# Kernel tuning notes

Hardware: AMD Instinct MI355X
Metric: run time of the kernel (lower is better)

The kernel has to match this reference:

```python
import jax, jax.numpy as jnp
import numpy as np

B, T, C = 4, 2048, 1024
H, D = 16, 64           # num_heads, head_size
R = D // 2              # rotary_ndims = 32


def _make_rope(T, R):
    # RotaryEmbedding(dim=R): inv_freq over arange(0, R, 2)
    inv_freq = 1.0 / (10000.0 ** (np.arange(0, R, 2, dtype=np.float32) / R))
    t = np.arange(T, dtype=np.float32)
    freqs = np.einsum('i,j->ij', t, inv_freq)        # [T, R/2]
    emb = np.concatenate([freqs, freqs], axis=-1)    # [T, R]
    return jnp.asarray(np.stack([np.cos(emb), np.sin(emb)]), dtype=jnp.float32)  # [2, T, R]


def setup_inputs() -> dict:
    key = jax.random.key(0)
    ks = jax.random.split(key, 10)
    s = 1.0 / np.sqrt(C)
    inp = {
        'x': jax.random.normal(ks[0], (B, T, C), dtype=jnp.float32),
        'RoPE': _make_rope(T, R),
        'key_padding_mask': jax.random.randint(ks[1], (B, T), 0, 2, dtype=jnp.int32),
        'Wq': jax.random.normal(ks[2], (C, C), dtype=jnp.float32) * s,
        'bq': jnp.zeros((C,), dtype=jnp.float32),
        'Wk': jax.random.normal(ks[3], (C, C), dtype=jnp.float32) * s,
        'bk': jnp.zeros((C,), dtype=jnp.float32),
        'Wv': jax.random.normal(ks[4], (C, C), dtype=jnp.float32) * s,
        'bv': jnp.zeros((C,), dtype=jnp.float32),
        'Wo': jax.random.normal(ks[5], (C, C), dtype=jnp.float32) * s,
        'bo': jnp.zeros((C,), dtype=jnp.float32),
    }
    return inp


def _rotate_half(x):
    x1, x2 = x[..., : x.shape[-1] // 2], x[..., x.shape[-1] // 2:]
    return jnp.concatenate([-x2, x1], axis=-1)


def reference(x, RoPE, key_padding_mask, Wq, bq, Wk, bk, Wv, bv, Wo, bo):
    Bx, Tx, Cx = x.shape
    # projections -> [B, H, T, D]
    def proj(W, b):
        return (x @ W.T + b).reshape(Bx, Tx, H, D).transpose(0, 2, 1, 3)
    q, k, v = proj(Wq, bq), proj(Wk, bk), proj(Wv, bv)

    # partial rotary: first R dims rotated, rest passed through
    q_rot, q_pass = q[..., :R], q[..., R:]
    k_rot, k_pass = k[..., :R], k[..., R:]
    cos, sin = RoPE[0][:Tx], RoPE[1][:Tx]            # [T, R]
    q_rot = q_rot * cos + _rotate_half(q_rot) * sin
    k_rot = k_rot * cos + _rotate_half(k_rot) * sin
    q = jnp.concatenate([q_rot, q_pass], axis=-1)
    k = jnp.concatenate([k_rot, k_pass], axis=-1)

    att = jnp.einsum('bhqd,bhkd->bhqk', q, k) * (1.0 / np.sqrt(D))
    mask = key_padding_mask[:, None, None, :]        # [B,1,1,T]
    att = jnp.where(mask == 0, jnp.asarray(-1e30, att.dtype), att)
    att = jax.nn.softmax(att, axis=-1)
    out = jnp.einsum('bhqk,bhkd->bhqd', att, v)      # [B,H,T,D]
    out = out.transpose(0, 2, 1, 3).reshape(Bx, Tx, Cx)
    return out @ Wo.T + bo
```

## Files before the change

kernel.cpp:

```cpp
#include <hip/hip_runtime.h>
#include <stdint.h>


typedef __attribute__((ext_vector_type(8))) short bf16x8;
typedef __attribute__((ext_vector_type(4))) float f32x4;
typedef __attribute__((ext_vector_type(4))) short short4v;
typedef __attribute__((ext_vector_type(4))) float float4v;
typedef __attribute__((ext_vector_type(2))) uint32_t uint2v;

#define MFMA16(a, b, c) __builtin_amdgcn_mfma_f32_16x16x32_bf16((a), (b), (c), 0, 0, 0)

#if __has_builtin(__builtin_amdgcn_exp2f)
#define FEXP(x) __builtin_amdgcn_exp2f(x)
#define QSCALE 0.18033688011112042f
#else
#define FEXP(x) __expf(x)
#define QSCALE 0.125f
#endif

static __device__ __forceinline__ short f2bf(float f) {
  union { float fv; uint32_t u; } v; v.fv = f;
  uint32_t r = v.u + 0x7FFFu + ((v.u >> 16) & 1u);
  return (short)(r >> 16);
}

static __device__ __forceinline__ uint32_t pack_trunc(float a, float b) {
  union { float f; uint32_t u; } ua, ub;
  ua.f = a; ub.f = b;
#if __has_builtin(__builtin_amdgcn_perm)
  return __builtin_amdgcn_perm(ub.u, ua.u, 0x07060302u);
#else
  return (ub.u & 0xFFFF0000u) | (ua.u >> 16);
#endif
}

typedef __attribute__((address_space(1))) void as1_void;
typedef __attribute__((address_space(3))) void as3_void;
static __device__ __forceinline__ void gld_lds16(const void* g, void* l) {
  __builtin_amdgcn_global_load_lds((as1_void*)g, (as3_void*)l, 16, 0, 0);
}

__global__ __launch_bounds__(256) void cvt_kernel(
    const float* x, const float* wq, const float* wk, const float* wv,
    const float* wo,
    short* xb, short* wqb, short* wkb, short* wvb, short* wob) {
  int64_t g = (int64_t)blockIdx.x * 256 + threadIdx.x;
  const int64_t NX = 8388608 / 4, NW = 1048576 / 4;
  const float* src;
  short* dst;
  int64_t i;
  if (g < NX)               { src = x;  dst = xb;  i = g; }
  else if (g < NX + NW)     { src = wq; dst = wqb; i = g - NX; }
  else if (g < NX + 2 * NW) { src = wk; dst = wkb; i = g - NX - NW; }
  else if (g < NX + 3 * NW) { src = wv; dst = wvb; i = g - NX - 2 * NW; }
  else                      { src = wo; dst = wob; i = g - NX - 3 * NW; }
  float4 v = ((const float4*)src)[i];
  short4v o;
  o[0] = f2bf(v.x); o[1] = f2bf(v.y); o[2] = f2bf(v.z); o[3] = f2bf(v.w);
  *(short4v*)&dst[i * 4] = o;
}

__global__ __launch_bounds__(256) void qkv_gemm(
    const short* __restrict__ Xb,
    const short* __restrict__ Wq, const short* __restrict__ Wk,
    const short* __restrict__ Wv,
    const float* __restrict__ bq, const float* __restrict__ bk,
    const float* __restrict__ bv,
    const float* __restrict__ rope, const int* __restrict__ mask,
    short* __restrict__ Qh, short* __restrict__ Kh, short* __restrict__ Vt) {
  __shared__ __align__(16) short As[128 * 32];
  __shared__ __align__(16) short Bs[128 * 32];

  const int t = threadIdx.x;
  const int lane = t & 63;
  const int wave = t >> 6;
  const int c = lane & 15;
  const int quad = lane >> 4;
  const int m0 = blockIdx.x * 128;
  const int n0 = blockIdx.y * 128;
  const int mat = blockIdx.z;
  const short* Wg = (mat == 0) ? Wq : (mat == 1) ? Wk : Wv;
  const float* bias = (mat == 0) ? bq : (mat == 1) ? bk : bv;

  f32x4 zero4 = {0.f, 0.f, 0.f, 0.f};
  f32x4 acc[4][4];
#pragma unroll
  for (int i = 0; i < 4; ++i)
#pragma unroll
    for (int j = 0; j < 4; ++j) acc[i][j] = zero4;

  const int wm = wave & 1, wn = wave >> 1;

  const int srow = t >> 2;
  const int slc = (t & 3) ^ (srow & 3);
  const short* gA = Xb + (size_t)(m0 + srow) * 1024 + slc * 8;
  const short* gB = Wg + (size_t)(n0 + srow) * 1024 + slc * 8;
  short* lA = &As[t * 8];
  short* lB = &Bs[t * 8];

  for (int k0 = 0; k0 < 1024; k0 += 32) {
    gld_lds16(gA + k0, lA);
    gld_lds16(gA + k0 + 65536, lA + 2048);
    gld_lds16(gB + k0, lB);
    gld_lds16(gB + k0 + 65536, lB + 2048);
    __syncthreads();

    bf16x8 af[4], bfr[4];
#pragma unroll
    for (int i = 0; i < 4; ++i) {
      int mr = wm * 64 + i * 16 + c;
      af[i] = *(const bf16x8*)&As[mr * 32 + ((quad ^ (mr & 3)) * 8)];
      int nr = wn * 64 + i * 16 + c;
      bfr[i] = *(const bf16x8*)&Bs[nr * 32 + ((quad ^ (nr & 3)) * 8)];
    }
#pragma unroll
    for (int i = 0; i < 4; ++i)
#pragma unroll
      for (int j = 0; j < 4; ++j) acc[i][j] = MFMA16(af[i], bfr[j], acc[i][j]);
    __syncthreads();
  }

  const int nb = n0 + wn * 64;
  const int hcol = nb >> 6;
  float bj[4];
#pragma unroll
  for (int j = 0; j < 4; ++j) bj[j] = bias[nb + j * 16 + c];
  const int bidx = m0 >> 11;
  const int tbase = (m0 & 2047) + wm * 64 + quad * 4;
  const int* mrow = mask + bidx * 2048;

  if (mat < 2) {
    short* Og = (mat == 0) ? Qh : Kh;
    size_t hb = (size_t)(bidx * 16 + hcol) * 2048;
#pragma unroll
    for (int i = 0; i < 4; ++i) {
#pragma unroll
      for (int r = 0; r < 4; ++r) {
        int tp = tbase + i * 16 + r;
        float f = (mat == 0) ? QSCALE : (mrow[tp] ? 1.0f : 0.0f);
        float cosv = rope[tp * 32 + c];
        float sinv = rope[65536 + tp * 32 + c];
        float v0 = acc[i][0][r] + bj[0];
        float v1 = acc[i][1][r] + bj[1];
        float v2 = acc[i][2][r] + bj[2];
        float v3 = acc[i][3][r] + bj[3];
        size_t base = (hb + tp) * 64;
        Og[base + c]      = f2bf((v0 * cosv - v1 * sinv) * f);
        Og[base + 16 + c] = f2bf((v1 * cosv + v0 * sinv) * f);
        Og[base + 32 + c] = f2bf(v2 * f);
        Og[base + 48 + c] = f2bf(v3 * f);
      }
    }
  } else {
    size_t hb = (size_t)(bidx * 16 + hcol) * 64;
#pragma unroll
    for (int i = 0; i < 4; ++i) {
      int tp = tbase + i * 16;
      int4 mv = *(const int4*)&mrow[tp];
      float fr[4];
      fr[0] = mv.x ? 1.f : 0.f; fr[1] = mv.y ? 1.f : 0.f;
      fr[2] = mv.z ? 1.f : 0.f; fr[3] = mv.w ? 1.f : 0.f;
#pragma unroll
      for (int j = 0; j < 4; ++j) {
        short4v pv;
#pragma unroll
        for (int r = 0; r < 4; ++r) pv[r] = f2bf((acc[i][j][r] + bj[j]) * fr[r]);
        size_t base = (hb + j * 16 + c) * 2048 + tp;
        *(short4v*)&Vt[base] = pv;
      }
    }
  }
}

__global__ __launch_bounds__(256, 4) void attn_kernel(
    const short* __restrict__ Qh, const short* __restrict__ Kh,
    const short* __restrict__ Vt, const int* __restrict__ mask,
    short* __restrict__ Og) {
  __shared__ __align__(16) short Ks[64 * 64];
  __shared__ __align__(16) short Vs[64 * 64];
  __shared__ __align__(16) short Pl[4][32 * 64];
  __shared__ float nmw[4];

  const int t = threadIdx.x;
  const int lane = t & 63;
  const int wave = t >> 6;
  const int c = lane & 15;
  const int quad = lane >> 4;
  const int qt = blockIdx.x;
  const int bh = blockIdx.y;
  const int bidx = bh >> 4;
  const short* Qg = Qh + ((size_t)bh * 2048 + qt * 128) * 64;
  const short* Kg = Kh + (size_t)bh * 2048 * 64;
  const short* Vg = Vt + (size_t)bh * 64 * 2048;

  {
    const int4* mr = (const int4*)(mask + bidx * 2048);
    int4 a = mr[t * 2], b = mr[t * 2 + 1];
    int cnt = (a.x == 0) + (a.y == 0) + (a.z == 0) + (a.w == 0) +
              (b.x == 0) + (b.y == 0) + (b.z == 0) + (b.w == 0);
    cnt += __shfl_xor(cnt, 1);  cnt += __shfl_xor(cnt, 2);
    cnt += __shfl_xor(cnt, 4);  cnt += __shfl_xor(cnt, 8);
    cnt += __shfl_xor(cnt, 16); cnt += __shfl_xor(cnt, 32);
    if (lane == 0) nmw[wave] = (float)cnt;
  }

  bf16x8 qf[2][2];
#pragma unroll
  for (int ks = 0; ks < 2; ++ks)
#pragma unroll
    for (int it = 0; it < 2; ++it)
      qf[ks][it] =
          *(const bf16x8*)&Qg[(wave * 32 + it * 16 + c) * 64 + ks * 32 + quad * 8];

  f32x4 zero4 = {0.f, 0.f, 0.f, 0.f};
  f32x4 O[4][2];
#pragma unroll
  for (int dt = 0; dt < 4; ++dt)
#pragma unroll
    for (int it = 0; it < 2; ++it) O[dt][it] = zero4;
  float l[2] = {0.f, 0.f};

  const int krow0 = t >> 3;
  const int klc = (t & 7) ^ (krow0 & 7);
  const short* gk0 = Kg + (size_t)krow0 * 64 + klc * 8;
  const short* gv0 = Vg + (size_t)krow0 * 2048 + klc * 8;
  short* Pw = &Pl[wave][0];

  for (int c0 = 0; c0 < 2048; c0 += 64) {
    gld_lds16(gk0 + (size_t)c0 * 64, &Ks[t * 8]);
    gld_lds16(gk0 + (size_t)(c0 + 32) * 64, &Ks[t * 8 + 2048]);
    gld_lds16(gv0 + c0, &Vs[t * 8]);
    gld_lds16(gv0 + c0 + 32 * 2048, &Vs[t * 8 + 2048]);
    __syncthreads();

    f32x4 St[4][2];
#pragma unroll
    for (int jt = 0; jt < 4; ++jt) { St[jt][0] = zero4; St[jt][1] = zero4; }
#pragma unroll
    for (int ks = 0; ks < 2; ++ks)
#pragma unroll
      for (int jt = 0; jt < 4; ++jt) {
        bf16x8 ak =
            *(const bf16x8*)&Ks[(jt * 16 + c) * 64 + (((4 * ks + quad) ^ (c & 7)) * 8)];
        St[jt][0] = MFMA16(ak, qf[ks][0], St[jt][0]);
        St[jt][1] = MFMA16(ak, qf[ks][1], St[jt][1]);
      }

#pragma unroll
    for (int it = 0; it < 2; ++it) {
#pragma unroll
      for (int jt = 0; jt < 4; ++jt) {
        float p0 = FEXP(St[jt][it][0]);
        float p1 = FEXP(St[jt][it][1]);
        float p2 = FEXP(St[jt][it][2]);
        float p3 = FEXP(St[jt][it][3]);
        l[it] += (p0 + p1) + (p2 + p3);
        uint2v pk;
        pk[0] = pack_trunc(p0, p1);
        pk[1] = pack_trunc(p2, p3);
        *(uint2v*)&Pw[(it * 16 + c) * 64 +
                      (((jt * 2 + (quad >> 1)) ^ (c & 7)) * 8) + (quad & 1) * 4] = pk;
      }
    }
    asm volatile("s_waitcnt lgkmcnt(0)" ::: "memory");

#pragma unroll
    for (int ks = 0; ks < 2; ++ks) {
      bf16x8 bp0 = *(const bf16x8*)&Pw[c * 64 + (((ks * 4 + quad) ^ (c & 7)) * 8)];
      bf16x8 bp1 =
          *(const bf16x8*)&Pw[(16 + c) * 64 + (((ks * 4 + quad) ^ (c & 7)) * 8)];
#pragma unroll
      for (int dt = 0; dt < 4; ++dt) {
        bf16x8 av =
            *(const bf16x8*)&Vs[(dt * 16 + c) * 64 + (((4 * ks + quad) ^ (c & 7)) * 8)];
        O[dt][0] = MFMA16(av, bp0, O[dt][0]);
        O[dt][1] = MFMA16(av, bp1, O[dt][1]);
      }
    }
    __syncthreads();
  }

  float nm = nmw[0] + nmw[1] + nmw[2] + nmw[3];
#pragma unroll
  for (int it = 0; it < 2; ++it) {
    float li = l[it];
    li += __shfl_xor(li, 16);
    li += __shfl_xor(li, 32);
    float inv = 1.0f / (li - nm);
    int tq = qt * 128 + wave * 32 + it * 16 + c;
    size_t rb = ((size_t)bidx * 2048 + tq) * 1024 + (size_t)(bh & 15) * 64;
#pragma unroll
    for (int dt = 0; dt < 4; ++dt) {
      short4v ov;
#pragma unroll
      for (int r = 0; r < 4; ++r) ov[r] = f2bf(O[dt][it][r] * inv);
      *(short4v*)&Og[rb + dt * 16 + quad * 4] = ov;
    }
  }
}

__global__ __launch_bounds__(256) void out_gemm(
    const short* __restrict__ Ab, const short* __restrict__ Wob,
    const float* __restrict__ bo, float* __restrict__ out) {
  __shared__ __align__(16) short As[128 * 32];
  __shared__ __align__(16) short Bs[128 * 32];

  const int t = threadIdx.x;
  const int lane = t & 63;
  const int wave = t >> 6;
  const int c = lane & 15;
  const int quad = lane >> 4;
  const int m0 = blockIdx.x * 128;
  const int n0 = blockIdx.y * 128;

  f32x4 zero4 = {0.f, 0.f, 0.f, 0.f};
  f32x4 acc[4][4];
#pragma unroll
  for (int i = 0; i < 4; ++i)
#pragma unroll
    for (int j = 0; j < 4; ++j) acc[i][j] = zero4;

  const int wm = wave & 1, wn = wave >> 1;
  const int srow = t >> 2;
  const int slc = (t & 3) ^ (srow & 3);
  const short* gA = Ab + (size_t)(m0 + srow) * 1024 + slc * 8;
  const short* gB = Wob + (size_t)(n0 + srow) * 1024 + slc * 8;
  short* lA = &As[t * 8];
  short* lB = &Bs[t * 8];

  for (int k0 = 0; k0 < 1024; k0 += 32) {
    gld_lds16(gA + k0, lA);
    gld_lds16(gA + k0 + 65536, lA + 2048);
    gld_lds16(gB + k0, lB);
    gld_lds16(gB + k0 + 65536, lB + 2048);
    __syncthreads();

    bf16x8 af[4], bfr[4];
#pragma unroll
    for (int i = 0; i < 4; ++i) {
      int mr = wm * 64 + i * 16 + c;
      af[i] = *(const bf16x8*)&As[mr * 32 + ((quad ^ (mr & 3)) * 8)];
      int nr = wn * 64 + i * 16 + c;
      bfr[i] = *(const bf16x8*)&Bs[nr * 32 + ((quad ^ (nr & 3)) * 8)];
    }
#pragma unroll
    for (int i = 0; i < 4; ++i)
#pragma unroll
      for (int j = 0; j < 4; ++j) acc[i][j] = MFMA16(af[i], bfr[j], acc[i][j]);
    __syncthreads();
  }

  const int nb = n0 + wn * 64;
  float bj[4];
#pragma unroll
  for (int j = 0; j < 4; ++j) bj[j] = bo[nb + j * 16 + c];
#pragma unroll
  for (int i = 0; i < 4; ++i) {
    int m = m0 + wm * 64 + i * 16 + quad * 4;
#pragma unroll
    for (int r = 0; r < 4; ++r) {
      float* orow = out + (size_t)(m + r) * 1024 + nb;
      orow[c]      = acc[i][0][r] + bj[0];
      orow[16 + c] = acc[i][1][r] + bj[1];
      orow[32 + c] = acc[i][2][r] + bj[2];
      orow[48 + c] = acc[i][3][r] + bj[3];
    }
  }
}

extern "C" void kernel_launch(void* const* d_in, const int* in_sizes, int n_in,
                              void* d_out, int out_size, void* d_ws,
                              size_t ws_size, hipStream_t stream) {
  const float* x    = (const float*)d_in[0];
  const float* rope = (const float*)d_in[1];
  const int*   mask = (const int*)d_in[2];
  const float* Wq   = (const float*)d_in[3];
  const float* bq   = (const float*)d_in[4];
  const float* Wk   = (const float*)d_in[5];
  const float* bk   = (const float*)d_in[6];
  const float* Wv   = (const float*)d_in[7];
  const float* bv   = (const float*)d_in[8];
  const float* Wo   = (const float*)d_in[9];
  const float* bo   = (const float*)d_in[10];
  float* out = (float*)d_out;

  char* ws = (char*)d_ws;
  short* xb  = (short*)(ws);
  short* wqb = (short*)(ws + 16777216);
  short* wkb = (short*)(ws + 18874368);
  short* wvb = (short*)(ws + 20971520);
  short* wob = (short*)(ws + 23068672);
  short* Qh  = (short*)(ws + 25198592);
  short* Kh  = (short*)(ws + 41975808);
  short* Vt  = (short*)(ws + 58753024);
  short* att = xb;

  cvt_kernel<<<12288, 256, 0, stream>>>(x, Wq, Wk, Wv, Wo, xb, wqb, wkb, wvb,
                                        wob);
  qkv_gemm<<<dim3(64, 8, 3), 256, 0, stream>>>(xb, wqb, wkb, wvb, bq, bk, bv,
                                               rope, mask, Qh, Kh, Vt);
  attn_kernel<<<dim3(16, 64), 256, 0, stream>>>(Qh, Kh, Vt, mask, att);
  out_gemm<<<dim3(64, 8), 256, 0, stream>>>(att, wob, bo, out);
}
```

Before: 292.0 us.

## Deepen GEMM K-tiles, shrink out_gemm M-tile, compute softmax row sums via MFMA

The QKV GEMM now stages 64-wide K slices with an 8-way XOR swizzle, which halves the number of barriers per K loop. The output GEMM switches to 64x128 tiles with a 4x2 MFMA accumulator per wave and doubles the grid, giving more blocks to fill the CUs. In attention, the per-thread softmax denominator sums and their cross-lane shuffles are replaced by an extra MFMA against a ones vector, and the S computation is split into two explicit passes. The cost is more LDS per block and extra MFMA work, and the row sums now come from the bf16-truncated P values instead of the fp32 exponentials.

```diff
diff --git a/kernel.cpp b/kernel.cpp
--- a/kernel.cpp
+++ b/kernel.cpp
@@ -5,7 +5,6 @@
 typedef __attribute__((ext_vector_type(8))) short bf16x8;
 typedef __attribute__((ext_vector_type(4))) float f32x4;
 typedef __attribute__((ext_vector_type(4))) short short4v;
-typedef __attribute__((ext_vector_type(4))) float float4v;
 typedef __attribute__((ext_vector_type(2))) uint32_t uint2v;
 
 #define MFMA16(a, b, c) __builtin_amdgcn_mfma_f32_16x16x32_bf16((a), (b), (c), 0, 0, 0)
@@ -68,8 +67,8 @@
     const float* __restrict__ bv,
     const float* __restrict__ rope, const int* __restrict__ mask,
     short* __restrict__ Qh, short* __restrict__ Kh, short* __restrict__ Vt) {
-  __shared__ __align__(16) short As[128 * 32];
-  __shared__ __align__(16) short Bs[128 * 32];
+  __shared__ __align__(16) short As[128 * 64];
+  __shared__ __align__(16) short Bs[128 * 64];
 
   const int t = threadIdx.x;
   const int lane = t & 63;
@@ -91,32 +90,34 @@
 
   const int wm = wave & 1, wn = wave >> 1;
 
-  const int srow = t >> 2;
-  const int slc = (t & 3) ^ (srow & 3);
-  const short* gA = Xb + (size_t)(m0 + srow) * 1024 + slc * 8;
-  const short* gB = Wg + (size_t)(n0 + srow) * 1024 + slc * 8;
-  short* lA = &As[t * 8];
-  short* lB = &Bs[t * 8];
-
-  for (int k0 = 0; k0 < 1024; k0 += 32) {
-    gld_lds16(gA + k0, lA);
-    gld_lds16(gA + k0 + 65536, lA + 2048);
-    gld_lds16(gB + k0, lB);
-    gld_lds16(gB + k0 + 65536, lB + 2048);
-    __syncthreads();
-
-    bf16x8 af[4], bfr[4];
-#pragma unroll
-    for (int i = 0; i < 4; ++i) {
-      int mr = wm * 64 + i * 16 + c;
-      af[i] = *(const bf16x8*)&As[mr * 32 + ((quad ^ (mr & 3)) * 8)];
-      int nr = wn * 64 + i * 16 + c;
-      bfr[i] = *(const bf16x8*)&Bs[nr * 32 + ((quad ^ (nr & 3)) * 8)];
-    }
-#pragma unroll
-    for (int i = 0; i < 4; ++i)
-#pragma unroll
-      for (int j = 0; j < 4; ++j) acc[i][j] = MFMA16(af[i], bfr[j], acc[i][j]);
+  const int srow = t >> 3;
+  const int schunk = (t & 7) ^ (srow & 7);
+  const short* gA = Xb + (size_t)(m0 + srow) * 1024 + schunk * 8;
+  const short* gB = Wg + (size_t)(n0 + srow) * 1024 + schunk * 8;
+
+  for (int k0 = 0; k0 < 1024; k0 += 64) {
+#pragma unroll
+    for (int cc = 0; cc < 4; ++cc) {
+      gld_lds16(gA + k0 + cc * 32 * 1024, &As[cc * 2048 + t * 8]);
+      gld_lds16(gB + k0 + cc * 32 * 1024, &Bs[cc * 2048 + t * 8]);
+    }
+    __syncthreads();
+
+#pragma unroll
+    for (int sl = 0; sl < 2; ++sl) {
+      bf16x8 af[4], bfr[4];
+#pragma unroll
+      for (int i = 0; i < 4; ++i) {
+        int mr = wm * 64 + i * 16 + c;
+        af[i] = *(const bf16x8*)&As[mr * 64 + (((sl * 4 + quad) ^ (mr & 7)) * 8)];
+        int nr = wn * 64 + i * 16 + c;
+        bfr[i] = *(const bf16x8*)&Bs[nr * 64 + (((sl * 4 + quad) ^ (nr & 7)) * 8)];
+      }
+#pragma unroll
+      for (int i = 0; i < 4; ++i)
+#pragma unroll
+        for (int j = 0; j < 4; ++j) acc[i][j] = MFMA16(af[i], bfr[j], acc[i][j]);
+    }
     __syncthreads();
   }
 
@@ -212,13 +213,16 @@
       qf[ks][it] =
           *(const bf16x8*)&Qg[(wave * 32 + it * 16 + c) * 64 + ks * 32 + quad * 8];
 
+  const bf16x8 ones = {0x3F80, 0x3F80, 0x3F80, 0x3F80,
+                       0x3F80, 0x3F80, 0x3F80, 0x3F80};
+
   f32x4 zero4 = {0.f, 0.f, 0.f, 0.f};
   f32x4 O[4][2];
 #pragma unroll
   for (int dt = 0; dt < 4; ++dt)
 #pragma unroll
     for (int it = 0; it < 2; ++it) O[dt][it] = zero4;
-  float l[2] = {0.f, 0.f};
+  f32x4 Ol[2] = {zero4, zero4};
 
   const int krow0 = t >> 3;
   const int klc = (t & 7) ^ (krow0 & 7);
@@ -235,16 +239,19 @@
 
     f32x4 St[4][2];
 #pragma unroll
-    for (int jt = 0; jt < 4; ++jt) { St[jt][0] = zero4; St[jt][1] = zero4; }
-#pragma unroll
-    for (int ks = 0; ks < 2; ++ks)
-#pragma unroll
-      for (int jt = 0; jt < 4; ++jt) {
-        bf16x8 ak =
-            *(const bf16x8*)&Ks[(jt * 16 + c) * 64 + (((4 * ks + quad) ^ (c & 7)) * 8)];
-        St[jt][0] = MFMA16(ak, qf[ks][0], St[jt][0]);
-        St[jt][1] = MFMA16(ak, qf[ks][1], St[jt][1]);
-      }
+    for (int jt = 0; jt < 4; ++jt) {
+      bf16x8 ak =
+          *(const bf16x8*)&Ks[(jt * 16 + c) * 64 + ((quad ^ (c & 7)) * 8)];
+      St[jt][0] = MFMA16(ak, qf[0][0], zero4);
+      St[jt][1] = MFMA16(ak, qf[0][1], zero4);
+    }
+#pragma unroll
+    for (int jt = 0; jt < 4; ++jt) {
+      bf16x8 ak =
+          *(const bf16x8*)&Ks[(jt * 16 + c) * 64 + (((4 + quad) ^ (c & 7)) * 8)];
+      St[jt][0] = MFMA16(ak, qf[1][0], St[jt][0]);
+      St[jt][1] = MFMA16(ak, qf[1][1], St[jt][1]);
+    }
 
 #pragma unroll
     for (int it = 0; it < 2; ++it) {
@@ -254,7 +261,6 @@
         float p1 = FEXP(St[jt][it][1]);
         float p2 = FEXP(St[jt][it][2]);
         float p3 = FEXP(St[jt][it][3]);
-        l[it] += (p0 + p1) + (p2 + p3);
         uint2v pk;
         pk[0] = pack_trunc(p0, p1);
         pk[1] = pack_trunc(p2, p3);
@@ -269,6 +275,8 @@
       bf16x8 bp0 = *(const bf16x8*)&Pw[c * 64 + (((ks * 4 + quad) ^ (c & 7)) * 8)];
       bf16x8 bp1 =
           *(const bf16x8*)&Pw[(16 + c) * 64 + (((ks * 4 + quad) ^ (c & 7)) * 8)];
+      Ol[0] = MFMA16(ones, bp0, Ol[0]);
+      Ol[1] = MFMA16(ones, bp1, Ol[1]);
 #pragma unroll
       for (int dt = 0; dt < 4; ++dt) {
         bf16x8 av =
@@ -283,10 +291,7 @@
   float nm = nmw[0] + nmw[1] + nmw[2] + nmw[3];
 #pragma unroll
   for (int it = 0; it < 2; ++it) {
-    float li = l[it];
-    li += __shfl_xor(li, 16);
-    li += __shfl_xor(li, 32);
-    float inv = 1.0f / (li - nm);
+    float inv = 1.0f / (Ol[it][0] - nm);
     int tq = qt * 128 + wave * 32 + it * 16 + c;
     size_t rb = ((size_t)bidx * 2048 + tq) * 1024 + (size_t)(bh & 15) * 64;
 #pragma unroll
@@ -302,68 +307,72 @@
 __global__ __launch_bounds__(256) void out_gemm(
     const short* __restrict__ Ab, const short* __restrict__ Wob,
     const float* __restrict__ bo, float* __restrict__ out) {
-  __shared__ __align__(16) short As[128 * 32];
-  __shared__ __align__(16) short Bs[128 * 32];
+  __shared__ __align__(16) short As[64 * 64];
+  __shared__ __align__(16) short Bs[128 * 64];
 
   const int t = threadIdx.x;
   const int lane = t & 63;
   const int wave = t >> 6;
   const int c = lane & 15;
   const int quad = lane >> 4;
-  const int m0 = blockIdx.x * 128;
+  const int m0 = blockIdx.x * 64;
   const int n0 = blockIdx.y * 128;
 
   f32x4 zero4 = {0.f, 0.f, 0.f, 0.f};
-  f32x4 acc[4][4];
-#pragma unroll
-  for (int i = 0; i < 4; ++i)
-#pragma unroll
-    for (int j = 0; j < 4; ++j) acc[i][j] = zero4;
-
-  const int wm = wave & 1, wn = wave >> 1;
-  const int srow = t >> 2;
-  const int slc = (t & 3) ^ (srow & 3);
-  const short* gA = Ab + (size_t)(m0 + srow) * 1024 + slc * 8;
-  const short* gB = Wob + (size_t)(n0 + srow) * 1024 + slc * 8;
-  short* lA = &As[t * 8];
-  short* lB = &Bs[t * 8];
-
-  for (int k0 = 0; k0 < 1024; k0 += 32) {
-    gld_lds16(gA + k0, lA);
-    gld_lds16(gA + k0 + 65536, lA + 2048);
-    gld_lds16(gB + k0, lB);
-    gld_lds16(gB + k0 + 65536, lB + 2048);
-    __syncthreads();
-
-    bf16x8 af[4], bfr[4];
-#pragma unroll
-    for (int i = 0; i < 4; ++i) {
-      int mr = wm * 64 + i * 16 + c;
-      af[i] = *(const bf16x8*)&As[mr * 32 + ((quad ^ (mr & 3)) * 8)];
-      int nr = wn * 64 + i * 16 + c;
-      bfr[i] = *(const bf16x8*)&Bs[nr * 32 + ((quad ^ (nr & 3)) * 8)];
-    }
-#pragma unroll
-    for (int i = 0; i < 4; ++i)
-#pragma unroll
-      for (int j = 0; j < 4; ++j) acc[i][j] = MFMA16(af[i], bfr[j], acc[i][j]);
-    __syncthreads();
-  }
-
-  const int nb = n0 + wn * 64;
-  float bj[4];
-#pragma unroll
-  for (int j = 0; j < 4; ++j) bj[j] = bo[nb + j * 16 + c];
+  f32x4 acc[4][2];
 #pragma unroll
   for (int i = 0; i < 4; ++i) {
-    int m = m0 + wm * 64 + i * 16 + quad * 4;
+    acc[i][0] = zero4;
+    acc[i][1] = zero4;
+  }
+
+  const int srow = t >> 3;
+  const int schunk = (t & 7) ^ (srow & 7);
+  const short* gA = Ab + (size_t)(m0 + srow) * 1024 + schunk * 8;
+  const short* gB = Wob + (size_t)(n0 + srow) * 1024 + schunk * 8;
+
+  for (int k0 = 0; k0 < 1024; k0 += 64) {
+    gld_lds16(gA + k0, &As[t * 8]);
+    gld_lds16(gA + k0 + 32 * 1024, &As[2048 + t * 8]);
+#pragma unroll
+    for (int cc = 0; cc < 4; ++cc)
+      gld_lds16(gB + k0 + cc * 32 * 1024, &Bs[cc * 2048 + t * 8]);
+    __syncthreads();
+
+#pragma unroll
+    for (int sl = 0; sl < 2; ++sl) {
+      bf16x8 af[4], bfr[2];
+#pragma unroll
+      for (int i = 0; i < 4; ++i) {
+        int mr = i * 16 + c;
+        af[i] = *(const bf16x8*)&As[mr * 64 + (((sl * 4 + quad) ^ (mr & 7)) * 8)];
+      }
+#pragma unroll
+      for (int j = 0; j < 2; ++j) {
+        int nr = wave * 32 + j * 16 + c;
+        bfr[j] = *(const bf16x8*)&Bs[nr * 64 + (((sl * 4 + quad) ^ (nr & 7)) * 8)];
+      }
+#pragma unroll
+      for (int i = 0; i < 4; ++i) {
+        acc[i][0] = MFMA16(af[i], bfr[0], acc[i][0]);
+        acc[i][1] = MFMA16(af[i], bfr[1], acc[i][1]);
+      }
+    }
+    __syncthreads();
+  }
+
+  const int nb = n0 + wave * 32;
+  float bj[2];
+  bj[0] = bo[nb + c];
+  bj[1] = bo[nb + 16 + c];
+#pragma unroll
+  for (int i = 0; i < 4; ++i) {
+    int m = m0 + i * 16 + quad * 4;
 #pragma unroll
     for (int r = 0; r < 4; ++r) {
       float* orow = out + (size_t)(m + r) * 1024 + nb;
       orow[c]      = acc[i][0][r] + bj[0];
       orow[16 + c] = acc[i][1][r] + bj[1];
-      orow[32 + c] = acc[i][2][r] + bj[2];
-      orow[48 + c] = acc[i][3][r] + bj[3];
     }
   }
 }
@@ -400,5 +409,5 @@
   qkv_gemm<<<dim3(64, 8, 3), 256, 0, stream>>>(xb, wqb, wkb, wvb, bq, bk, bv,
                                                rope, mask, Qh, Kh, Vt);
   attn_kernel<<<dim3(16, 64), 256, 0, stream>>>(Qh, Kh, Vt, mask, att);
-  out_gemm<<<dim3(64, 8), 256, 0, stream>>>(att, wob, bo, out);
-}
+  out_gemm<<<dim3(128, 8), 256, 0, stream>>>(att, wob, bo, out);
+}
```

Result: slower. 325.6 us (+11.5%).
